# Optimization experiments

Measured on AMD Instinct MI355X. Metric: run time of the kernel, lower is better.

## Reference

```python
import jax, jax.numpy as jnp
import numpy as np

B = 32768      # batch
D = 512        # embedding dim
V = 100000     # vocab_length (row 0 reserved -> table has V+1 rows)
S = 100        # num_neg_samples (hard-coded in source)
DISTORTION = 0.4


def _expected_counts():
    # fixed_unigram sampler: zipf-ish counts, distorted by 0.4, 1 reserved id
    counts = 1.0 / np.arange(1, V + 1, dtype=np.float64)
    p = counts ** DISTORTION
    p = p / p.sum()
    q = np.zeros(V + 1, dtype=np.float64)
    # unique sampling expected count: E[id in sample] = 1-(1-p)^S
    q[1:] = -np.expm1(S * np.log1p(-p))
    q[0] = 1e-9  # reserved id, never sampled; avoid log(0)
    return q


def setup_inputs() -> dict:
    key = jax.random.key(0)
    k1, k2, k3, k4 = jax.random.split(key, 4)
    label = jax.random.randint(k1, (B,), 1, V + 1, dtype=jnp.int64)
    inputs = jax.random.normal(k2, (B, D), dtype=jnp.float32)
    weights = jax.random.normal(k3, (V + 1, D), dtype=jnp.float32) * 0.05
    biases = jnp.zeros((V + 1,), dtype=jnp.float32)
    sampled_ids = jax.random.choice(k4, V, (S,), replace=False).astype(jnp.int64) + 1
    q = jnp.asarray(_expected_counts(), dtype=jnp.float32)
    true_expected_count = q[label]          # [B]
    sampled_expected_count = q[sampled_ids]  # [S]
    return {
        "label": label, "inputs": inputs, "weights": weights, "biases": biases,
        "sampled_ids": sampled_ids,
        "true_expected_count": true_expected_count,
        "sampled_expected_count": sampled_expected_count,
    }


def reference(label, inputs, weights, biases, sampled_ids,
              true_expected_count, sampled_expected_count):
    # --- _compute_sampled_logits with subtract_log_q=True ---
    true_w = weights[label]                                   # [B, D] gather
    true_logits = (jnp.einsum('bd,bd->b', inputs, true_w)
                   + biases[label]
                   - jnp.log(true_expected_count))            # [B]
    samp_w = weights[sampled_ids]                             # [S, D] gather
    samp_logits = (jnp.einsum('bd,sd->bs', inputs, samp_w)
                   + biases[sampled_ids]
                   - jnp.log(sampled_expected_count))         # [B, S]
    logits = jnp.concatenate([true_logits[:, None], samp_logits], axis=1)  # [B, 1+S]
    # labels are one-hot at column 0 -> CE = logsumexp - true logit
    losses = jax.nn.logsumexp(logits, axis=1) - logits[:, 0]
    loss = jnp.mean(losses)
    return logits, loss
```

## Files before the change

### kernel.cpp

```cpp
#include <hip/hip_runtime.h>
#include <math.h>

#define B_TOT 32768
#define DIM   512
#define NS    100
#define NCOL  101
#define TB    128
#define NBLK  (B_TOT / TB)
#define WPITCH 520

typedef __attribute__((ext_vector_type(8))) short short8;
typedef __attribute__((ext_vector_type(4))) float f32x4;

static __device__ __forceinline__ short f2bf(float f) {
    unsigned u = __builtin_bit_cast(unsigned, f);
    unsigned r = (u + 0x7FFFu + ((u >> 16) & 1u)) >> 16;
    return (short)r;
}

__global__ __launch_bounds__(512)
void fused_kernel(const int* __restrict__ label,
                  const float* __restrict__ inputs,
                  const float* __restrict__ weights,
                  const float* __restrict__ biases,
                  const int* __restrict__ sids,
                  const float* __restrict__ tq,
                  const float* __restrict__ sq,
                  float* __restrict__ out,
                  float* __restrict__ lpart)
{
    __shared__ short W_lds[112 * WPITCH];
    __shared__ float base_lds[112];
    __shared__ int   s_sid[NS];
    __shared__ float ls_lds[8];

    const int t = threadIdx.x;

    if (t < NS) s_sid[t] = sids[t];
    __syncthreads();

    for (int idx = t; idx < NS * 128; idx += 512) {
        const int row = idx >> 7;
        const int kq  = (idx & 127) * 4;
        const float4 wv = *(const float4*)(weights + (long)s_sid[row] * DIM + kq);
        *(short4*)&W_lds[row * WPITCH + kq] =
            make_short4(f2bf(wv.x), f2bf(wv.y), f2bf(wv.z), f2bf(wv.w));
    }
    for (int idx = t; idx < 12 * (WPITCH / 4); idx += 512) {
        const int row = 100 + idx / (WPITCH / 4);
        const int kq  = (idx % (WPITCH / 4)) * 4;
        *(short4*)&W_lds[row * WPITCH + kq] = make_short4(0, 0, 0, 0);
    }
    if (t < 112)
        base_lds[t] = (t < NS) ? biases[s_sid[t]] - logf(sq[t]) : -INFINITY;

    const int wave = t >> 6;
    const int lane = t & 63;
    const int rit  = lane & 15;
    const int seg  = lane >> 4;
    const long b0  = (long)blockIdx.x * TB;
    const long absRow = b0 + wave * 16 + rit;
    const int lab = label[absRow];
    const float* aptr = inputs  + absRow * DIM + seg * 8;
    const float* wtp  = weights + (long)lab * DIM + seg * 8;

    f32x4 acc_r[7];
    #pragma unroll
    for (int c = 0; c < 7; c++) acc_r[c] = (f32x4){0.f, 0.f, 0.f, 0.f};

    float4 ar[4][2];
    float4 wr[8][2];
    #pragma unroll
    for (int p = 0; p < 4; p++) {
        ar[p][0] = *(const float4*)(aptr + p * 32);
        ar[p][1] = *(const float4*)(aptr + p * 32 + 4);
    }
    #pragma unroll
    for (int p = 0; p < 8; p++) {
        wr[p][0] = *(const float4*)(wtp + p * 32);
        wr[p][1] = *(const float4*)(wtp + p * 32 + 4);
    }

    __syncthreads();

    float t0 = 0.f, t1 = 0.f;
    #pragma unroll
    for (int kc = 0; kc < 16; kc++) {
        const int sa = kc & 3, sw = kc & 7;
        const float4 a0 = ar[sa][0], a1 = ar[sa][1];
        const float4 w0 = wr[sw][0], w1 = wr[sw][1];
        if (kc + 4 < 16) {
            ar[sa][0] = *(const float4*)(aptr + (kc + 4) * 32);
            ar[sa][1] = *(const float4*)(aptr + (kc + 4) * 32 + 4);
        }
        if (kc + 8 < 16) {
            wr[sw][0] = *(const float4*)(wtp + (kc + 8) * 32);
            wr[sw][1] = *(const float4*)(wtp + (kc + 8) * 32 + 4);
        }

        t0 = fmaf(a0.x, w0.x, t0); t0 = fmaf(a0.y, w0.y, t0);
        t0 = fmaf(a0.z, w0.z, t0); t0 = fmaf(a0.w, w0.w, t0);
        t1 = fmaf(a1.x, w1.x, t1); t1 = fmaf(a1.y, w1.y, t1);
        t1 = fmaf(a1.z, w1.z, t1); t1 = fmaf(a1.w, w1.w, t1);

        short8 af;
        af[0] = f2bf(a0.x); af[1] = f2bf(a0.y); af[2] = f2bf(a0.z); af[3] = f2bf(a0.w);
        af[4] = f2bf(a1.x); af[5] = f2bf(a1.y); af[6] = f2bf(a1.z); af[7] = f2bf(a1.w);

        const int wko = kc * 32 + seg * 8;
        #pragma unroll
        for (int c = 0; c < 7; c++) {
            const short8 bf = *(const short8*)&W_lds[(c * 16 + rit) * WPITCH + wko];
            acc_r[c] = __builtin_amdgcn_mfma_f32_16x16x32_bf16(af, bf, acc_r[c], 0, 0, 0);
        }
    }
    float tacc = t0 + t1;

    tacc += __shfl_xor(tacc, 16);
    tacc += __shfl_xor(tacc, 32);
    const float tl = tacc + biases[lab] - logf(tq[absRow]);
    if (lane < 16) out[absRow * NCOL] = tl;

    const int g = lane >> 4;
    float base_v[7];
    #pragma unroll
    for (int c = 0; c < 7; c++) base_v[c] = base_lds[c * 16 + rit];

    float loss_sum = 0.f;
    #pragma unroll
    for (int i = 0; i < 4; i++) {
        const int r = g * 4 + i;
        const long orow = (b0 + wave * 16 + r) * NCOL;
        const float tlv = __shfl(tl, r);
        float v[7];
        float m = tlv;
        #pragma unroll
        for (int c = 0; c < 7; c++) {
            v[c] = acc_r[c][i] + base_v[c];
            m = fmaxf(m, v[c]);
        }
        #pragma unroll
        for (int off = 1; off < 16; off <<= 1) m = fmaxf(m, __shfl_xor(m, off));
        float s = (rit == 0) ? expf(tlv - m) : 0.f;
        #pragma unroll
        for (int c = 0; c < 7; c++) s += expf(v[c] - m);
        #pragma unroll
        for (int off = 1; off < 16; off <<= 1) s += __shfl_xor(s, off);
        loss_sum += m + logf(s) - tlv;
        #pragma unroll
        for (int c = 0; c < 7; c++) {
            const int col = c * 16 + rit;
            if (col < NS) out[orow + 1 + col] = v[c];
        }
    }
    float wl = (rit == 0) ? loss_sum : 0.f;
    wl += __shfl_xor(wl, 16);
    wl += __shfl_xor(wl, 32);
    if (lane == 0) ls_lds[wave] = wl;
    __syncthreads();
    if (t == 0) {
        float bp = 0.f;
        #pragma unroll
        for (int w = 0; w < 8; w++) bp += ls_lds[w];
        lpart[blockIdx.x] = bp;
    }
}

__global__ __launch_bounds__(256)
void reduce_kernel(const float* __restrict__ lpart, float* __restrict__ out_loss)
{
    __shared__ double buf[256];
    buf[threadIdx.x] = (double)lpart[threadIdx.x];
    __syncthreads();
    for (int o = 128; o > 0; o >>= 1) {
        if (threadIdx.x < o) buf[threadIdx.x] += buf[threadIdx.x + o];
        __syncthreads();
    }
    if (threadIdx.x == 0) *out_loss = (float)(buf[0] * (1.0 / (double)B_TOT));
}

extern "C" void kernel_launch(void* const* d_in, const int* in_sizes, int n_in,
                              void* d_out, int out_size, void* d_ws, size_t ws_size,
                              hipStream_t stream)
{
    const int*   label   = (const int*)d_in[0];
    const float* inputs  = (const float*)d_in[1];
    const float* weights = (const float*)d_in[2];
    const float* biases  = (const float*)d_in[3];
    const int*   sids    = (const int*)d_in[4];
    const float* tq      = (const float*)d_in[5];
    const float* sq      = (const float*)d_in[6];
    float* out   = (float*)d_out;
    float* lpart = (float*)d_ws;

    fused_kernel<<<NBLK, 512, 0, stream>>>(label, inputs, weights, biases,
                                           sids, tq, sq, out, lpart);
    reduce_kernel<<<1, 256, 0, stream>>>(lpart, out + (long)B_TOT * NCOL);
}
```

Measured before the change: 38.52 us.

## Fuse final loss reduction into main kernel via last-block ticket

Removes the separate reduce kernel launch. Each block now bumps a global atomic ticket after writing its partial loss, and the last block to arrive sums all partials in shared memory. The ticket is zeroed with a memset on the same stream. The change also swaps the order of the weight and input prefetch loads and replaces __syncthreads with a bare barrier after waiting only on LDS counters, so the global prefetch loads can stay in flight across the barrier.

```diff
diff --git a/kernel.cpp b/kernel.cpp
--- a/kernel.cpp
+++ b/kernel.cpp
@@ -27,12 +27,15 @@
                   const float* __restrict__ tq,
                   const float* __restrict__ sq,
                   float* __restrict__ out,
-                  float* __restrict__ lpart)
+                  float* __restrict__ lpart,
+                  unsigned* __restrict__ ticket)
 {
     __shared__ short W_lds[112 * WPITCH];
     __shared__ float base_lds[112];
     __shared__ int   s_sid[NS];
     __shared__ float ls_lds[8];
+    __shared__ unsigned lastf;
+    __shared__ double dbuf[NBLK];
 
     const int t = threadIdx.x;
 
@@ -68,20 +71,21 @@
     #pragma unroll
     for (int c = 0; c < 7; c++) acc_r[c] = (f32x4){0.f, 0.f, 0.f, 0.f};
 
+    float4 wr[8][2];
     float4 ar[4][2];
-    float4 wr[8][2];
+    #pragma unroll
+    for (int p = 0; p < 8; p++) {
+        wr[p][0] = *(const float4*)(wtp + p * 32);
+        wr[p][1] = *(const float4*)(wtp + p * 32 + 4);
+    }
     #pragma unroll
     for (int p = 0; p < 4; p++) {
         ar[p][0] = *(const float4*)(aptr + p * 32);
         ar[p][1] = *(const float4*)(aptr + p * 32 + 4);
     }
-    #pragma unroll
-    for (int p = 0; p < 8; p++) {
-        wr[p][0] = *(const float4*)(wtp + p * 32);
-        wr[p][1] = *(const float4*)(wtp + p * 32 + 4);
-    }
-
-    __syncthreads();
+
+    asm volatile("s_waitcnt lgkmcnt(0)" ::: "memory");
+    __builtin_amdgcn_s_barrier();
 
     float t0 = 0.f, t1 = 0.f;
     #pragma unroll
@@ -89,13 +93,13 @@
         const int sa = kc & 3, sw = kc & 7;
         const float4 a0 = ar[sa][0], a1 = ar[sa][1];
         const float4 w0 = wr[sw][0], w1 = wr[sw][1];
+        if (kc + 8 < 16) {
+            wr[sw][0] = *(const float4*)(wtp + (kc + 8) * 32);
+            wr[sw][1] = *(const float4*)(wtp + (kc + 8) * 32 + 4);
+        }
         if (kc + 4 < 16) {
             ar[sa][0] = *(const float4*)(aptr + (kc + 4) * 32);
             ar[sa][1] = *(const float4*)(aptr + (kc + 4) * 32 + 4);
-        }
-        if (kc + 8 < 16) {
-            wr[sw][0] = *(const float4*)(wtp + (kc + 8) * 32);
-            wr[sw][1] = *(const float4*)(wtp + (kc + 8) * 32 + 4);
         }
 
         t0 = fmaf(a0.x, w0.x, t0); t0 = fmaf(a0.y, w0.y, t0);
@@ -158,25 +162,28 @@
     wl += __shfl_xor(wl, 32);
     if (lane == 0) ls_lds[wave] = wl;
     __syncthreads();
+
     if (t == 0) {
         float bp = 0.f;
         #pragma unroll
         for (int w = 0; w < 8; w++) bp += ls_lds[w];
         lpart[blockIdx.x] = bp;
-    }
-}
-
-__global__ __launch_bounds__(256)
-void reduce_kernel(const float* __restrict__ lpart, float* __restrict__ out_loss)
-{
-    __shared__ double buf[256];
-    buf[threadIdx.x] = (double)lpart[threadIdx.x];
+        __threadfence();
+        const unsigned old = atomicAdd(ticket, 1u);
+        lastf = (old == NBLK - 1) ? 1u : 0u;
+    }
     __syncthreads();
-    for (int o = 128; o > 0; o >>= 1) {
-        if (threadIdx.x < o) buf[threadIdx.x] += buf[threadIdx.x + o];
+    if (lastf) {
+        __threadfence();
+        if (t < NBLK) dbuf[t] = (double)lpart[t];
         __syncthreads();
-    }
-    if (threadIdx.x == 0) *out_loss = (float)(buf[0] * (1.0 / (double)B_TOT));
+        for (int o = NBLK / 2; o > 0; o >>= 1) {
+            if (t < o) dbuf[t] += dbuf[t + o];
+            __syncthreads();
+        }
+        if (t == 0)
+            out[(long)B_TOT * NCOL] = (float)(dbuf[0] * (1.0 / (double)B_TOT));
+    }
 }
 
 extern "C" void kernel_launch(void* const* d_in, const int* in_sizes, int n_in,
@@ -190,10 +197,11 @@
     const int*   sids    = (const int*)d_in[4];
     const float* tq      = (const float*)d_in[5];
     const float* sq      = (const float*)d_in[6];
-    float* out   = (float*)d_out;
-    float* lpart = (float*)d_ws;
-
+    float* out      = (float*)d_out;
+    float* lpart    = (float*)d_ws;
+    unsigned* ticket = (unsigned*)((char*)d_ws + 1024);
+
+    hipMemsetAsync(ticket, 0, 4, stream);
     fused_kernel<<<NBLK, 512, 0, stream>>>(label, inputs, weights, biases,
-                                           sids, tq, sq, out, lpart);
-    reduce_kernel<<<1, 256, 0, stream>>>(lpart, out + (long)B_TOT * NCOL);
+                                           sids, tq, sq, out, lpart, ticket);
 }
```

After: 51.56 us. +33.9%, slower.
